# Optimization experiments

Measured on AMD Instinct MI355X. Metric: run time of the kernel, lower is better.

## Reference

```python
import jax, jax.numpy as jnp
import numpy as np

WIN_H, WIN_W = 8, 16
N = WIN_H * WIN_W            # 128 tokens per window
DIM, HEADS = 512, 16
TOW = 64 // WIN_H            # type_of_windows = input_resolution[0] // window_size[0] = 8
B_WIN = 2048                 # number of windows (B_)


def _earth_position_index():
    # Faithful port of get_earth_position_index (torch wraps negative indices;
    # we pre-wrap with mod so the gather uses nonnegative indices identically).
    ch = np.arange(WIN_H)
    cw = np.arange(WIN_W)
    coords = np.stack(np.meshgrid(ch, cw, indexing='ij'))        # [2, h, w]
    cf = coords.reshape(2, -1)                                   # [2, N]
    rel = cf[:, :, None] - cf[:, None, :]                        # [2, N, N]
    rel = rel.transpose(1, 2, 0).copy()                          # [N, N, 2]
    rel[:, :, 0] *= 2 * WIN_W - 1
    rel[:, :, 1] += WIN_W - 1
    idx = rel.sum(-1)                                            # [N, N], may be negative
    table_len = WIN_H ** 2 * (2 * WIN_W - 1)                     # 1984
    return (idx % table_len).astype(np.int32)


def setup_inputs() -> dict:
    key = jax.random.key(0)
    ks = jax.random.split(key, 6)
    table_len = WIN_H ** 2 * (2 * WIN_W - 1)
    inv_sqrt_dim = 1.0 / np.sqrt(DIM)
    return {
        'x': jax.random.normal(ks[0], (B_WIN, N, DIM), dtype=jnp.float32),
        'qkv_w': jax.random.normal(ks[1], (3 * DIM, DIM), dtype=jnp.float32) * inv_sqrt_dim,
        'qkv_b': jax.random.normal(ks[2], (3 * DIM,), dtype=jnp.float32) * 0.02,
        'proj_w': jax.random.normal(ks[3], (DIM, DIM), dtype=jnp.float32) * inv_sqrt_dim,
        'proj_b': jax.random.normal(ks[4], (DIM,), dtype=jnp.float32) * 0.02,
        'bias_table': jax.random.normal(ks[5], (table_len, TOW, HEADS), dtype=jnp.float32) * 0.02,
        'pos_index': jnp.asarray(_earth_position_index()),
    }


def reference(x, qkv_w, qkv_b, proj_w, proj_b, bias_table, pos_index):
    B_, Nn, C = x.shape
    hd = C // HEADS
    scale = hd ** (-0.5)
    # fused QKV projection: [B_, N, 3, H, hd]
    qkv = (x @ qkv_w.T + qkv_b).reshape(B_, Nn, 3, HEADS, hd)
    q = qkv[:, :, 0].transpose(0, 2, 1, 3) * scale               # [B_, H, N, hd]
    k = qkv[:, :, 1].transpose(0, 2, 1, 3)
    v = qkv[:, :, 2].transpose(0, 2, 1, 3)
    attn = jnp.einsum('bhnd,bhmd->bhnm', q, k)                   # [B_, H, N, N]
    # earth position bias: gather [N*N] rows -> [N, N, TOW, H], pick middle latitude
    epb = bias_table[pos_index.reshape(-1)].reshape(Nn, Nn, TOW, HEADS)
    epb = epb[:, :, TOW // 2, :]                                 # [N, N, H]
    attn = attn + epb.transpose(2, 0, 1)[None]                   # + [1, H, N, N]
    attn = jax.nn.softmax(attn, axis=-1)
    out = jnp.einsum('bhnm,bhmd->bhnd', attn, v)                 # [B_, H, N, hd]
    out = out.transpose(0, 2, 1, 3).reshape(B_, Nn, C)
    return out @ proj_w.T + proj_b
```

## Files before the change

kernel.cpp:

```cpp
#include <hip/hip_runtime.h>
#include <hip/hip_bf16.h>


typedef short short8 __attribute__((ext_vector_type(8)));
typedef float f32x4 __attribute__((ext_vector_type(4)));
typedef unsigned short u16;
typedef unsigned int u32;

__device__ __forceinline__ u16 f2bf(float f) {
    __bf16 h = (__bf16)f;
    union { __bf16 b; u16 u; } v; v.b = h;
    return v.u;
}

__device__ __forceinline__ f32x4 mfma16(short8 a, short8 b, f32x4 c) {
    return __builtin_amdgcn_mfma_f32_16x16x32_bf16(a, b, c, 0, 0, 0);
}

#define GLDS16(gsrc, ldst)                                                  \
    __builtin_amdgcn_global_load_lds(                                       \
        (const __attribute__((address_space(1))) void*)(gsrc),              \
        (__attribute__((address_space(3))) void*)(ldst), 16, 0, 0)

__global__ __launch_bounds__(256) void cvt_x_kernel(
    const float4* __restrict__ xin, int4* __restrict__ xbf)
{
    int idx = blockIdx.x * 256 + threadIdx.x;
    for (; idx < 16777216; idx += 8192 * 256) {
        const float4 a = xin[idx * 2], b = xin[idx * 2 + 1];
        int4 o;
        o.x = (u32)f2bf(a.x) | ((u32)f2bf(a.y) << 16);
        o.y = (u32)f2bf(a.z) | ((u32)f2bf(a.w) << 16);
        o.z = (u32)f2bf(b.x) | ((u32)f2bf(b.y) << 16);
        o.w = (u32)f2bf(b.z) | ((u32)f2bf(b.w) << 16);
        xbf[idx] = o;
    }
}

__global__ __launch_bounds__(256) void prep_kernel(
    const float* __restrict__ qkv_w, const float* __restrict__ proj_w,
    const float* __restrict__ btab, const int* __restrict__ pidx,
    u16* __restrict__ qkvw_bf, u16* __restrict__ projw_bf,
    float* __restrict__ epb)
{
    const int i = blockIdx.x * 256 + threadIdx.x;
    qkvw_bf[i] = f2bf(qkv_w[i]);
    if (i < 512 * 512) projw_bf[i] = f2bf(proj_w[i]);
    if (i < 16 * 128 * 128) {
        const int rc = i & 16383, h = i >> 14;
        epb[i] = btab[pidx[rc] * 128 + 64 + h];
    }
}


template<bool EPI_QKV>
__global__ __launch_bounds__(256) void gemm_bt(
    const u16* __restrict__ A, const u16* __restrict__ Bt,
    const float* __restrict__ bias, void* __restrict__ Cv,
    u16* __restrict__ kb, u16* __restrict__ vtb,
    const int Nn, const int K, const float qscale)
{
    __shared__ __attribute__((aligned(16))) char sm[32768];

    const int tid = threadIdx.x;
    const int lane = tid & 63;
    const int w = tid >> 6;
    const int lo = lane & 15, g = lane >> 4;
    const int wm = w >> 1, wn = w & 1;
    const int wofs = __builtin_amdgcn_readfirstlane(w) * 1024;
    const int ntile = Nn >> 7;

    int wg = blockIdx.x;
    {
        const int cpx = gridDim.x >> 3;
        wg = (wg & 7) * cpx + (wg >> 3);
    }
    const int bm = wg / ntile, bn = wg % ntile;
    const size_t m0 = (size_t)bm << 7;
    const int n0 = bn << 7;
    const int nk = K >> 5;

    const int rs = tid >> 2;
    const int c8 = (((tid & 3) ^ ((tid >> 3) & 3))) * 8;
    const u16* pa0 = A + (m0 + rs) * (size_t)K + c8;
    const u16* pa1 = pa0 + (size_t)64 * K;
    const u16* pb0 = Bt + (size_t)(n0 + rs) * K + c8;
    const u16* pb1 = pb0 + (size_t)64 * K;

#define STAGE(buf, kt)                                                     \
    do {                                                                   \
        const int ko = (kt) << 5;                                          \
        char* d = sm + (buf) * 16384 + wofs;                               \
        GLDS16(pa0 + ko, d);                                               \
        GLDS16(pa1 + ko, d + 4096);                                        \
        GLDS16(pb0 + ko, d + 8192);                                        \
        GLDS16(pb1 + ko, d + 12288);                                       \
    } while (0)

    f32x4 acc[4][4] = {};

    STAGE(0, 0);
    asm volatile("s_waitcnt vmcnt(0)" ::: "memory");
    __builtin_amdgcn_s_barrier();

    const int csw16 = (g ^ ((lo >> 1) & 3)) << 4;

    int buf = 0;
    for (int t = 0; t < nk; ++t) {
        if (t + 1 < nk) STAGE(buf ^ 1, t + 1);
        const char* Ab = sm + buf * 16384;
        const char* Bb = Ab + 8192;
        short8 af[4], bq[4];
#pragma unroll
        for (int i = 0; i < 4; ++i) {
            af[i] = *(const short8*)(Ab + (wm * 64 + i * 16 + lo) * 64 + csw16);
            bq[i] = *(const short8*)(Bb + (wn * 64 + i * 16 + lo) * 64 + csw16);
        }
#pragma unroll
        for (int i = 0; i < 4; ++i)
#pragma unroll
            for (int j = 0; j < 4; ++j)
                acc[i][j] = mfma16(af[i], bq[j], acc[i][j]);
        asm volatile("s_waitcnt vmcnt(0)" ::: "memory");
        asm volatile("" ::: "memory");
        __builtin_amdgcn_s_barrier();
        buf ^= 1;
    }
#undef STAGE

    if constexpr (EPI_QKV) {
        u16* Ct = (u16*)sm;
        const int b16 = ((int)(m0 >> 7)) * 16;
        const int tsel = bn >> 2;
        const int h0 = (bn & 3) << 2;
        u16* outb = (tsel == 0) ? (u16*)Cv : (tsel == 1) ? kb : vtb;
        if (tsel < 2) {
            const float sc = (tsel == 0) ? qscale : 1.0f;
#pragma unroll
            for (int ph = 0; ph < 2; ++ph) {
                __syncthreads();
                if (wm == ph) {
#pragma unroll
                    for (int j = 0; j < 4; ++j) {
                        const int c = wn * 64 + j * 16 + lo;
                        const float bv = bias[n0 + c];
#pragma unroll
                        for (int i = 0; i < 4; ++i)
#pragma unroll
                            for (int ii = 0; ii < 4; ++ii) {
                                const int r = i * 16 + g * 4 + ii;
                                Ct[r * 136 + c] = f2bf((acc[i][j][ii] + bv) * sc);
                            }
                    }
                }
                __syncthreads();
#pragma unroll
                for (int it = 0; it < 4; ++it) {
                    const int idx = it * 256 + tid;
                    const int r = idx >> 4, s2 = idx & 15;
                    const int hl = s2 >> 2, d0 = (s2 & 3) * 8;
                    *(int4*)(outb + ((size_t)(b16 + h0 + hl) * 128
                                     + ph * 64 + r) * 32 + d0) =
                        *(const int4*)(Ct + r * 136 + s2 * 8);
                }
            }
        } else {
#pragma unroll
            for (int ph = 0; ph < 2; ++ph) {
                __syncthreads();
                if (wn == ph) {
#pragma unroll
                    for (int j = 0; j < 4; ++j) {
                        const int c = j * 16 + lo;
                        const float bv = bias[n0 + ph * 64 + c];
#pragma unroll
                        for (int i = 0; i < 4; ++i)
#pragma unroll
                            for (int ii = 0; ii < 4; ++ii) {
                                const int r = wm * 64 + i * 16 + g * 4 + ii;
                                Ct[c * 136 + r] = f2bf(acc[i][j][ii] + bv);
                            }
                    }
                }
                __syncthreads();
#pragma unroll
                for (int it = 0; it < 4; ++it) {
                    const int idx = it * 256 + tid;
                    const int cidx = idx >> 4, nc = idx & 15;
                    const int gc = ph * 64 + cidx;
                    const int hl = gc >> 5, d = gc & 31;
                    *(int4*)(outb + ((size_t)(b16 + h0 + hl) * 32 + d) * 128
                             + nc * 8) =
                        *(const int4*)(Ct + cidx * 136 + nc * 8);
                }
            }
        }
    } else {
        float* Cg = (float*)Cv;
#pragma unroll
        for (int j = 0; j < 4; ++j) {
            const int c = wn * 64 + j * 16 + lo;
            const float bv = bias[n0 + c];
#pragma unroll
            for (int i = 0; i < 4; ++i)
#pragma unroll
                for (int ii = 0; ii < 4; ++ii) {
                    const size_t r = m0 + wm * 64 + i * 16 + g * 4 + ii;
                    Cg[r * (size_t)Nn + n0 + c] = acc[i][j][ii] + bv;
                }
        }
    }
}

__global__ __launch_bounds__(256) void attn_kernel(
    const u16* __restrict__ qbuf, const u16* __restrict__ kbuf,
    const u16* __restrict__ vtbuf, const float* __restrict__ epb,
    u16* __restrict__ aout)
{
    __shared__ __attribute__((aligned(16))) char smem[43520];
    u16 (*Vt)[136]      = (u16(*)[136])smem;
    char* Qs            = smem + 8704;
    char* Ks            = smem + 16896;
    u16 (*Ps)[32][136]  = (u16(*)[32][136])(smem + 8704);
    u16 (*Os)[32]       = (u16(*)[32])smem;

    const int h = blockIdx.x >> 11;
    const int b = blockIdx.x & 2047;
    const int tid = threadIdx.x;
    const int lane = tid & 63, w = tid >> 6;
    const int lo = lane & 15, g = lane >> 4;
    const int wu = __builtin_amdgcn_readfirstlane(w);

    const size_t hb = (size_t)(b * 16 + h) * 4096;
    const u16* qp = qbuf + hb;
    const u16* kp = kbuf + hb;
    const u16* vp = vtbuf + hb;

    const int c8 = ((lane & 3) ^ ((lane >> 3) & 3)) * 8;
    const int rofs = (lane >> 2) * 32;
#pragma unroll
    for (int cc = 0; cc < 2; ++cc) {
        const int ch = wu * 2 + cc;
        GLDS16(qp + ch * 512 + rofs + c8, Qs + ch * 1024);
        GLDS16(kp + ch * 512 + rofs + c8, Ks + ch * 1024);
    }
#pragma unroll
    for (int it = 0; it < 2; ++it) {
        const int idx = tid + it * 256;
        const int d = idx >> 4, nc = idx & 15;
        const int4 v = *(const int4*)(vp + idx * 8);
        *(int4*)(&Vt[d][nc * 8]) = v;
    }
    __syncthreads();

    const int r0 = w * 32;
    const int csw16 = (g ^ ((lo >> 1) & 3)) << 4;

    short8 aq[2], bk[8];
    aq[0] = *(const short8*)(Qs + (r0 + lo) * 64 + csw16);
    aq[1] = *(const short8*)(Qs + (r0 + 16 + lo) * 64 + csw16);
#pragma unroll
    for (int j = 0; j < 8; ++j)
        bk[j] = *(const short8*)(Ks + (j * 16 + lo) * 64 + csw16);

    f32x4 acc[2][8];
#pragma unroll
    for (int j = 0; j < 8; ++j) {
        f32x4 z = {0.f, 0.f, 0.f, 0.f};
        acc[0][j] = mfma16(aq[0], bk[j], z);
        acc[1][j] = mfma16(aq[1], bk[j], z);
    }

    const float* eb = epb + (h << 14);
    float mrow[2][4], rsum[2][4];
#pragma unroll
    for (int mt = 0; mt < 2; ++mt)
#pragma unroll
        for (int ii = 0; ii < 4; ++ii) { mrow[mt][ii] = -1e30f; rsum[mt][ii] = 0.f; }

#pragma unroll
    for (int mt = 0; mt < 2; ++mt)
#pragma unroll
        for (int j = 0; j < 8; ++j)
#pragma unroll
            for (int ii = 0; ii < 4; ++ii) {
                const int r = r0 + mt * 16 + g * 4 + ii;
                const int c = j * 16 + lo;
                const float sv = acc[mt][j][ii] + eb[(r << 7) + c];
                acc[mt][j][ii] = sv;
                mrow[mt][ii] = fmaxf(mrow[mt][ii], sv);
            }
#pragma unroll
    for (int d = 1; d < 16; d <<= 1)
#pragma unroll
        for (int mt = 0; mt < 2; ++mt)
#pragma unroll
            for (int ii = 0; ii < 4; ++ii)
                mrow[mt][ii] = fmaxf(mrow[mt][ii], __shfl_xor(mrow[mt][ii], d, 64));

    __syncthreads();

#pragma unroll
    for (int mt = 0; mt < 2; ++mt)
#pragma unroll
        for (int j = 0; j < 8; ++j)
#pragma unroll
            for (int ii = 0; ii < 4; ++ii) {
                const float p = __expf(acc[mt][j][ii] - mrow[mt][ii]);
                rsum[mt][ii] += p;
                Ps[w][mt * 16 + g * 4 + ii][j * 16 + lo] = f2bf(p);
            }
#pragma unroll
    for (int d = 1; d < 16; d <<= 1)
#pragma unroll
        for (int mt = 0; mt < 2; ++mt)
#pragma unroll
            for (int ii = 0; ii < 4; ++ii)
                rsum[mt][ii] += __shfl_xor(rsum[mt][ii], d, 64);

    f32x4 o[2][2] = {};
#pragma unroll
    for (int kk = 0; kk < 4; ++kk) {
        short8 av[2];
        av[0] = *(const short8*)(&Ps[w][lo][kk * 32 + g * 8]);
        av[1] = *(const short8*)(&Ps[w][16 + lo][kk * 32 + g * 8]);
#pragma unroll
        for (int dt = 0; dt < 2; ++dt) {
            const short8 bv = *(const short8*)(&Vt[dt * 16 + lo][kk * 32 + g * 8]);
            o[0][dt] = mfma16(av[0], bv, o[0][dt]);
            o[1][dt] = mfma16(av[1], bv, o[1][dt]);
        }
    }

    __syncthreads();

#pragma unroll
    for (int mt = 0; mt < 2; ++mt)
#pragma unroll
        for (int dt = 0; dt < 2; ++dt)
#pragma unroll
            for (int ii = 0; ii < 4; ++ii)
                Os[r0 + mt * 16 + g * 4 + ii][dt * 16 + lo] =
                    f2bf(o[mt][dt][ii] / rsum[mt][ii]);
    __syncthreads();

    u16* op = aout + (size_t)b * 128 * 512 + h * 32;
#pragma unroll
    for (int it = 0; it < 2; ++it) {
        const int idx = tid + it * 256;
        const int r = idx >> 2, c = (idx & 3) * 8;
        *(int4*)(op + (size_t)r * 512 + c) = *(const int4*)(&Os[r][c]);
    }
}

extern "C" void kernel_launch(void* const* d_in, const int* in_sizes, int n_in,
                              void* d_out, int out_size, void* d_ws, size_t ws_size,
                              hipStream_t stream)
{
    const float* x      = (const float*)d_in[0];
    const float* qkv_w  = (const float*)d_in[1];
    const float* qkv_b  = (const float*)d_in[2];
    const float* proj_w = (const float*)d_in[3];
    const float* proj_b = (const float*)d_in[4];
    const float* btab   = (const float*)d_in[5];
    const int*   pidx   = (const int*)d_in[6];

    char* ws = (char*)d_ws;
    u16*   xbf      = (u16*)(ws);
    u16*   attnbuf  = (u16*)(ws);
    u16*   qkvw_bf  = (u16*)(ws + 268435456);
    u16*   projw_bf = (u16*)(ws + 270008320);
    float* epb      = (float*)(ws + 270532608);
    u16*   qbuf     = (u16*)(ws + 271581184);
    u16*   kbuf     = (u16*)(ws + 540016640);
    u16*   vtbuf    = (u16*)(ws + 808452096);

    const float qscale = 0.17677669529663687f;

    cvt_x_kernel<<<dim3(8192), dim3(256), 0, stream>>>(
        (const float4*)x, (int4*)xbf);

    prep_kernel<<<dim3(3072), dim3(256), 0, stream>>>(
        qkv_w, proj_w, btab, pidx, qkvw_bf, projw_bf, epb);

    gemm_bt<true><<<dim3(2048 * 12), dim3(256), 0, stream>>>(
        xbf, qkvw_bf, qkv_b, qbuf, kbuf, vtbuf, 1536, 512, qscale);

    attn_kernel<<<dim3(32768), dim3(256), 0, stream>>>(
        qbuf, kbuf, vtbuf, epb, attnbuf);

    gemm_bt<false><<<dim3(2048 * 4), dim3(256), 0, stream>>>(
        attnbuf, projw_bf, proj_b, d_out, nullptr, nullptr, 512, 512, 1.0f);
}
```

Before: 1.448 ms.

## Use single-buffered 64-wide K tiles in GEMM instead of double-buffered 32-wide

The GEMM main loop now stages a 128x64 K-slice of A and B per iteration into one LDS buffer, with an XOR swizzle over 8 16-byte chunks, and drops the double-buffered 32-wide scheme. This halves the number of loop iterations and barriers and doubles MFMA work per sync. The cost is that global loads no longer overlap compute: each tile load sits between two barriers, which exposes memory latency.

```diff
diff --git a/kernel.cpp b/kernel.cpp
--- a/kernel.cpp
+++ b/kernel.cpp
@@ -61,6 +61,8 @@
     const int Nn, const int K, const float qscale)
 {
     __shared__ __attribute__((aligned(16))) char sm[32768];
+    char* As = sm;
+    char* Bs = sm + 16384;
 
     const int tid = threadIdx.x;
     const int lane = tid & 63;
@@ -78,53 +80,56 @@
     const int bm = wg / ntile, bn = wg % ntile;
     const size_t m0 = (size_t)bm << 7;
     const int n0 = bn << 7;
-    const int nk = K >> 5;
-
-    const int rs = tid >> 2;
-    const int c8 = (((tid & 3) ^ ((tid >> 3) & 3))) * 8;
-    const u16* pa0 = A + (m0 + rs) * (size_t)K + c8;
-    const u16* pa1 = pa0 + (size_t)64 * K;
-    const u16* pb0 = Bt + (size_t)(n0 + rs) * K + c8;
-    const u16* pb1 = pb0 + (size_t)64 * K;
-
-#define STAGE(buf, kt)                                                     \
+    const int nk = K >> 6;
+
+    const u16* pa[4];
+    const u16* pb[4];
+#pragma unroll
+    for (int i = 0; i < 4; ++i) {
+        const int s = i * 256 + tid;
+        const int r = s >> 3, c16 = s & 7;
+        const int csw = (c16 ^ (r & 7)) << 3;
+        pa[i] = A + (m0 + r) * (size_t)K + csw;
+        pb[i] = Bt + (size_t)(n0 + r) * K + csw;
+    }
+
+#define STAGE(kt)                                                          \
     do {                                                                   \
-        const int ko = (kt) << 5;                                          \
-        char* d = sm + (buf) * 16384 + wofs;                               \
-        GLDS16(pa0 + ko, d);                                               \
-        GLDS16(pa1 + ko, d + 4096);                                        \
-        GLDS16(pb0 + ko, d + 8192);                                        \
-        GLDS16(pb1 + ko, d + 12288);                                       \
+        const int koff = (kt) * 64;                                        \
+        _Pragma("unroll")                                                  \
+        for (int i = 0; i < 4; ++i)                                        \
+            GLDS16(pa[i] + koff, As + i * 4096 + wofs);                    \
+        _Pragma("unroll")                                                  \
+        for (int i = 0; i < 4; ++i)                                        \
+            GLDS16(pb[i] + koff, Bs + i * 4096 + wofs);                    \
     } while (0)
 
     f32x4 acc[4][4] = {};
 
-    STAGE(0, 0);
-    asm volatile("s_waitcnt vmcnt(0)" ::: "memory");
-    __builtin_amdgcn_s_barrier();
-
-    const int csw16 = (g ^ ((lo >> 1) & 3)) << 4;
-
-    int buf = 0;
-    for (int t = 0; t < nk; ++t) {
-        if (t + 1 < nk) STAGE(buf ^ 1, t + 1);
-        const char* Ab = sm + buf * 16384;
-        const char* Bb = Ab + 8192;
-        short8 af[4], bq[4];
-#pragma unroll
-        for (int i = 0; i < 4; ++i) {
-            af[i] = *(const short8*)(Ab + (wm * 64 + i * 16 + lo) * 64 + csw16);
-            bq[i] = *(const short8*)(Bb + (wn * 64 + i * 16 + lo) * 64 + csw16);
+    STAGE(0);
+    for (int kt = 0;;) {
+        __syncthreads();
+#pragma unroll
+        for (int kk = 0; kk < 2; ++kk) {
+            short8 af[4], bq[4];
+            const int cb = (kk * 4 + g) << 4;
+            const int sz = (lo & 7) << 4;
+#pragma unroll
+            for (int i = 0; i < 4; ++i) {
+                const int ra = wm * 64 + i * 16 + lo;
+                af[i] = *(const short8*)(As + ((ra * 128 + cb) ^ sz));
+                const int rb = wn * 64 + i * 16 + lo;
+                bq[i] = *(const short8*)(Bs + ((rb * 128 + cb) ^ sz));
+            }
+#pragma unroll
+            for (int i = 0; i < 4; ++i)
+#pragma unroll
+                for (int j = 0; j < 4; ++j)
+                    acc[i][j] = mfma16(af[i], bq[j], acc[i][j]);
         }
-#pragma unroll
-        for (int i = 0; i < 4; ++i)
-#pragma unroll
-            for (int j = 0; j < 4; ++j)
-                acc[i][j] = mfma16(af[i], bq[j], acc[i][j]);
-        asm volatile("s_waitcnt vmcnt(0)" ::: "memory");
-        asm volatile("" ::: "memory");
-        __builtin_amdgcn_s_barrier();
-        buf ^= 1;
+        if (++kt == nk) break;
+        __syncthreads();
+        STAGE(kt);
     }
 #undef STAGE
 
```

Result: faster. 1.400 ms (-3.3%).
